# Performance work log

Measured on AMD Instinct MI355X. Metric: run time of the kernel, lower is better.

## Reference

```python
import jax, jax.numpy as jnp
import numpy as np

NP_, NA_, NS_ = 200000, 30000, 50000
D = 128          # embed_dim == hidden_dim
P = 128          # projection_dim
L = 3            # num GNN layers
R = 6            # num relations
LN_EPS = 1e-5
L2_EPS = 1e-12

# relation order matches metadata[1]: (src_type, dst_type, n_src, n_dst, n_edges)
RELS = [
    ("artist", "performance", NA_, NP_, 400000),      # performs
    ("performance", "song", NP_, NS_, 400000),        # performing
    ("artist", "song", NA_, NS_, 150000),             # composed
    ("performance", "artist", NP_, NA_, 400000),      # rev_performs
    ("song", "performance", NS_, NP_, 400000),        # rev_performing
    ("song", "artist", NS_, NA_, 150000),             # rev_composed
]
NNODES = {"performance": NP_, "artist": NA_, "song": NS_}


def _segment_mean(src, idx, n):
    # src: [E, D] messages, idx: [E] destination ids
    s = jax.ops.segment_sum(src, idx, num_segments=n)
    c = jax.ops.segment_sum(jnp.ones((src.shape[0], 1), src.dtype), idx, num_segments=n)
    return s / jnp.maximum(c, 1.0)


def _l2norm(x):
    n = jnp.linalg.norm(x, axis=-1, keepdims=True)
    return x / jnp.maximum(n, L2_EPS)


def _layernorm(x, g, b):
    mu = jnp.mean(x, axis=-1, keepdims=True)
    var = jnp.mean(jnp.square(x - mu), axis=-1, keepdims=True)
    return (x - mu) * jax.lax.rsqrt(var + LN_EPS) * g + b


def setup_inputs() -> dict:
    key = jax.random.key(0)
    ks = list(jax.random.split(key, 32))
    ki = iter(ks)
    inp = {}
    inp["perf_nid"] = jnp.arange(NP_, dtype=jnp.int32)
    inp["artist_nid"] = jnp.arange(NA_, dtype=jnp.int32)
    inp["song_nid"] = jnp.arange(NS_, dtype=jnp.int32)
    enames = ["e_performs", "e_performing", "e_composed",
              "e_rev_performs", "e_rev_performing", "e_rev_composed"]
    for name, (s, t, n_src, n_dst, n_e) in zip(enames, RELS):
        src = jax.random.randint(next(ki), (n_e,), 0, n_src, dtype=jnp.int32)
        dst = jax.random.randint(next(ki), (n_e,), 0, n_dst, dtype=jnp.int32)
        inp[name] = jnp.stack([src, dst])  # [2, E]
    inp["emb_performance"] = jax.random.normal(next(ki), (NP_, D), jnp.float32)
    inp["emb_artist"] = jax.random.normal(next(ki), (NA_, D), jnp.float32)
    inp["emb_song"] = jax.random.normal(next(ki), (NS_, D), jnp.float32)
    sc = 1.0 / np.sqrt(D)
    inp["Wl"] = jax.random.normal(next(ki), (L, R, D, D), jnp.float32) * sc
    inp["bl"] = jnp.zeros((L, R, D), jnp.float32)
    inp["Wr"] = jax.random.normal(next(ki), (L, R, D, D), jnp.float32) * sc
    inp["ln_g"] = jnp.ones((3, D), jnp.float32)
    inp["ln_b"] = jnp.zeros((3, D), jnp.float32)
    inp["pw1"] = jax.random.normal(next(ki), (3, D, P), jnp.float32) * sc
    inp["pb1"] = jnp.zeros((3, P), jnp.float32)
    inp["pw2"] = jax.random.normal(next(ki), (3, P, P), jnp.float32) * (1.0 / np.sqrt(P))
    inp["pb2"] = jnp.zeros((3, P), jnp.float32)
    return inp


def _forward(perf_nid, artist_nid, song_nid, edges,
             emb_performance, emb_artist, emb_song,
             Wl, bl, Wr, ln_g, ln_b, pw1, pb1, pw2, pb2):
    x = {
        "performance": emb_performance[perf_nid],
        "artist": emb_artist[artist_nid],
        "song": emb_song[song_nid],
    }
    for layer in range(L):
        new = {t: 0.0 for t in x}
        for r, ((s, t, _, _, _), e) in enumerate(zip(RELS, edges)):
            # SAGEConv: lin_l(mean_agg(x_src)) + lin_r(x_dst), then L2 normalize
            msg = _segment_mean(x[s][e[0]], e[1], x[t].shape[0])
            out = msg @ Wl[layer, r] + bl[layer, r] + x[t] @ Wr[layer, r]
            new[t] = new[t] + _l2norm(out)  # HeteroConv aggr='sum'
        x = new
        if layer < L - 1:
            x = {t: jax.nn.relu(v) for t, v in x.items()}
    res = []
    for i, t in enumerate(["performance", "artist", "song"]):
        h = _layernorm(x[t], ln_g[i], ln_b[i])
        h = jax.nn.relu(h @ pw1[i] + pb1[i]) @ pw2[i] + pb2[i]
        res.append(_l2norm(h))
    return tuple(res)


def reference(perf_nid, artist_nid, song_nid,
              e_performs, e_performing, e_composed,
              e_rev_performs, e_rev_performing, e_rev_composed,
              emb_performance, emb_artist, emb_song,
              Wl, bl, Wr, ln_g, ln_b, pw1, pb1, pw2, pb2):
    edges = [e_performs, e_performing, e_composed,
             e_rev_performs, e_rev_performing, e_rev_composed]
    return _forward(perf_nid, artist_nid, song_nid, edges,
                    emb_performance, emb_artist, emb_song,
                    Wl, bl, Wr, ln_g, ln_b, pw1, pb1, pw2, pb2)
```

## Files before the change

kernel.cpp:

```cpp
#include <hip/hip_runtime.h>
#include <math.h>


#define NPF 200000
#define NAR 30000
#define NSO 50000
#define NDTOT 560000
#define ETOT  1900000
#define VPT 12
#define SCAN_CHUNK (256 * VPT)
#define SCAN_NB 183

#define BLKP 3125
#define BLKA 469
#define BLKS 782
#define BLKTOT (BLKP + BLKA + BLKS)

typedef __attribute__((ext_vector_type(8))) short bf16x8;
typedef __attribute__((ext_vector_type(4))) float f32x4;

__device__ __forceinline__ unsigned short f2bf(float f) {
  union { float f; unsigned u; } v; v.f = f;
  unsigned u = v.u;
  u += 0x7FFFu + ((u >> 16) & 1u);
  return (unsigned short)(u >> 16);
}
__device__ __forceinline__ float bf2f(unsigned short h) {
  union { unsigned u; float f; } v; v.u = ((unsigned)h) << 16;
  return v.f;
}

struct BF3 { short h, m, l; };
__device__ __forceinline__ BF3 split3(float f) {
  BF3 r;
  unsigned short hh = f2bf(f);
  float r1 = f - bf2f(hh);
  unsigned short mm = f2bf(r1);
  float r2 = r1 - bf2f(mm);
  r.h = (short)hh; r.m = (short)mm; r.l = (short)f2bf(r2);
  return r;
}
struct BF2 { short h, m; };
__device__ __forceinline__ BF2 split2(float f) {
  BF2 r;
  unsigned short hh = f2bf(f);
  r.h = (short)hh;
  r.m = (short)f2bf(f - bf2f(hh));
  return r;
}

#define MFMA6(ah, am, al, bh, bm, blo, acc)                                     \
  acc = __builtin_amdgcn_mfma_f32_16x16x32_bf16(ah, bh, acc, 0, 0, 0);          \
  acc = __builtin_amdgcn_mfma_f32_16x16x32_bf16(am, bh, acc, 0, 0, 0);          \
  acc = __builtin_amdgcn_mfma_f32_16x16x32_bf16(ah, bm, acc, 0, 0, 0);          \
  acc = __builtin_amdgcn_mfma_f32_16x16x32_bf16(al, bh, acc, 0, 0, 0);          \
  acc = __builtin_amdgcn_mfma_f32_16x16x32_bf16(am, bm, acc, 0, 0, 0);          \
  acc = __builtin_amdgcn_mfma_f32_16x16x32_bf16(ah, blo, acc, 0, 0, 0);
#define MFMA3(ah, am, bh, bm, acc)                                              \
  acc = __builtin_amdgcn_mfma_f32_16x16x32_bf16(ah, bh, acc, 0, 0, 0);          \
  acc = __builtin_amdgcn_mfma_f32_16x16x32_bf16(am, bh, acc, 0, 0, 0);          \
  acc = __builtin_amdgcn_mfma_f32_16x16x32_bf16(ah, bm, acc, 0, 0, 0);

__device__ __forceinline__ void blk_decode(int b, int* t, int* lb) {
  if (b < BLKP)             { *t = 0; *lb = b; }
  else if (b < BLKP + BLKA) { *t = 1; *lb = b - BLKP; }
  else                      { *t = 2; *lb = b - BLKP - BLKA; }
}

__global__ void k_gather_all(const int* __restrict__ nidP, const int* __restrict__ nidA,
                             const int* __restrict__ nidS,
                             const float4* __restrict__ embP, const float4* __restrict__ embA,
                             const float4* __restrict__ embS, float4* __restrict__ dst) {
  int i = blockIdx.x * blockDim.x + threadIdx.x;
  if (i >= 280000 * 32) return;
  int r = i >> 5, c = i & 31;
  const int* nid; const float4* emb; int lr;
  if (r < NPF)            { nid = nidP; emb = embP; lr = r; }
  else if (r < NPF + NAR) { nid = nidA; emb = embA; lr = r - NPF; }
  else                    { nid = nidS; emb = embS; lr = r - NPF - NAR; }
  dst[(size_t)r * 32 + c] = emb[(size_t)nid[lr] * 32 + c];
}

__device__ __forceinline__ void edge_decode(int i,
    const int* e0, const int* e1, const int* e2, const int* e3, const int* e4, const int* e5,
    const int** eg, int* lo, int* E, int* co) {
  if (i < 400000)       { *eg = e0; *lo = i;           *E = 400000; *co = 0; }
  else if (i < 800000)  { *eg = e1; *lo = i - 400000;  *E = 400000; *co = 200000; }
  else if (i < 950000)  { *eg = e2; *lo = i - 800000;  *E = 150000; *co = 250000; }
  else if (i < 1350000) { *eg = e3; *lo = i - 950000;  *E = 400000; *co = 300000; }
  else if (i < 1750000) { *eg = e4; *lo = i - 1350000; *E = 400000; *co = 330000; }
  else                  { *eg = e5; *lo = i - 1750000; *E = 150000; *co = 530000; }
}

__global__ void k_count_all(const int* e0, const int* e1, const int* e2,
                            const int* e3, const int* e4, const int* e5,
                            int* __restrict__ cnt) {
  int i = blockIdx.x * blockDim.x + threadIdx.x;
  if (i >= ETOT) return;
  const int* eg; int lo, E, co;
  edge_decode(i, e0, e1, e2, e3, e4, e5, &eg, &lo, &E, &co);
  atomicAdd(&cnt[co + eg[E + lo]], 1);
}

__global__ void k_scan_block(const int* __restrict__ cnt, int n, int* __restrict__ part) {
  __shared__ int sd[256];
  int t = threadIdx.x;
  int base = blockIdx.x * SCAN_CHUNK + t * VPT;
  int s = 0;
#pragma unroll
  for (int i = 0; i < VPT; ++i) { int idx = base + i; if (idx < n) s += cnt[idx]; }
  sd[t] = s; __syncthreads();
  for (int off = 128; off > 0; off >>= 1) { if (t < off) sd[t] += sd[t + off]; __syncthreads(); }
  if (t == 0) part[blockIdx.x] = sd[0];
}

__global__ void k_scan_top(int* part, int nb) {
  __shared__ int sd[256];
  int t = threadIdx.x;
  int v = (t < nb) ? part[t] : 0;
  sd[t] = v; __syncthreads();
  for (int off = 1; off < 256; off <<= 1) {
    int add = (t >= off) ? sd[t - off] : 0;
    __syncthreads();
    sd[t] += add;
    __syncthreads();
  }
  if (t < nb) part[t] = sd[t] - v;
}

__global__ void k_scan_final(int* __restrict__ cnt, int n, const int* __restrict__ part,
                             int* __restrict__ rp, int E) {
  __shared__ int sd[256];
  int t = threadIdx.x;
  int base = blockIdx.x * SCAN_CHUNK + t * VPT;
  int v[VPT]; int s = 0;
#pragma unroll
  for (int i = 0; i < VPT; ++i) { int idx = base + i; v[i] = (idx < n) ? cnt[idx] : 0; s += v[i]; }
  sd[t] = s; __syncthreads();
  for (int off = 1; off < 256; off <<= 1) {
    int add = (t >= off) ? sd[t - off] : 0;
    __syncthreads();
    sd[t] += add;
    __syncthreads();
  }
  int run = part[blockIdx.x] + sd[t] - s;
#pragma unroll
  for (int i = 0; i < VPT; ++i) {
    int idx = base + i;
    if (idx < n) { rp[idx] = run; cnt[idx] = 0; }
    run += v[i];
  }
  if (blockIdx.x == 0 && t == 0) rp[n] = E;
}

__global__ void k_fill_all(const int* e0, const int* e1, const int* e2,
                           const int* e3, const int* e4, const int* e5,
                           const int* __restrict__ rp, int* __restrict__ cur,
                           int* __restrict__ col) {
  int i = blockIdx.x * blockDim.x + threadIdx.x;
  if (i >= ETOT) return;
  const int* eg; int lo, E, co;
  edge_decode(i, e0, e1, e2, e3, e4, e5, &eg, &lo, &E, &co);
  int d = co + eg[E + lo];
  int p = atomicAdd(&cur[d], 1);
  col[rp[d] + p] = eg[lo];
}

#define PKSTRIDE 49152
__global__ void k_packW(const float* __restrict__ Wl, const float* __restrict__ Wr,
                        const float* __restrict__ pw1, const float* __restrict__ pw2,
                        unsigned short* __restrict__ pk) {
  int gid = blockIdx.x * blockDim.x + threadIdx.x;
  if (gid >= 42 * 4 * 8 * 64) return;
  int lane = gid & 63;
  int t = (gid >> 6) & 7;
  int s = (gid >> 9) & 3;
  int m = gid >> 11;
  const float* src;
  if (m < 18) src = Wl + (size_t)m * 16384;
  else if (m < 36) src = Wr + (size_t)(m - 18) * 16384;
  else if (m < 39) src = pw1 + (size_t)(m - 36) * 16384;
  else src = pw2 + (size_t)(m - 39) * 16384;
  int n = t * 16 + (lane & 15);
  int k0 = s * 32 + (lane >> 4) * 8;
  unsigned short* hi = pk + (size_t)m * PKSTRIDE + ((size_t)(s * 8 + t) * 64 + lane) * 8;
  unsigned short* mid = hi + 16384;
  unsigned short* lo = hi + 32768;
#pragma unroll
  for (int j = 0; j < 8; ++j) {
    float f = src[(size_t)(k0 + j) * 128 + n];
    BF3 w = split3(f);
    hi[j] = (unsigned short)w.h;
    mid[j] = (unsigned short)w.m;
    lo[j] = (unsigned short)w.l;
  }
}

__global__ __launch_bounds__(256) void k_sage_merged(
    const int* __restrict__ rp, const int* __restrict__ col,
    const float* __restrict__ xin, float* __restrict__ xout,
    const unsigned short* __restrict__ pkw, const float* __restrict__ bl,
    int layer, int slot, int relu_out) {
  __shared__ float Ms[64 * 128];
  static const int RELSLOT[2][3] = {{0, 3, 1}, {4, 5, 2}};
  static const int SRCT[2][3]    = {{1, 0, 0}, {2, 2, 1}};
  static const int CNT_OFF[6] = {0, 200000, 250000, 300000, 330000, 530000};
  static const int TOFFc[3] = {0, NPF, NPF + NAR};
  static const int TNc[3]   = {NPF, NAR, NSO};
  int ty, lb;
  blk_decode(blockIdx.x, &ty, &lb);
  int rel = RELSLOT[slot][ty];
  int m = layer * 6 + rel;
  const int* rpt = rp + CNT_OFF[rel];
  const float* xsrc = xin + (size_t)TOFFc[SRCT[slot][ty]] * 128;
  const float* xdst = xin + (size_t)TOFFc[ty] * 128;
  float* outp = xout + (size_t)TOFFc[ty] * 128;
  const unsigned short* pkl = pkw + (size_t)m * PKSTRIDE;
  const unsigned short* pkr = pkw + (size_t)(18 + m) * PKSTRIDE;
  const float* blv = bl + (size_t)m * 128;
  int n_dst = TNc[ty];
  int first = (slot == 0);

  int lane = threadIdx.x & 63;
  int wave = threadIdx.x >> 6;
  int row0b = lb * 64;

  {
    int g = lane >> 4, li = lane & 15;
    int c0 = li * 8;
    int bb[4], ne[4];
    int maxd = 0;
#pragma unroll
    for (int i = 0; i < 4; ++i) {
      int d = row0b + wave * 16 + g * 4 + i;
      int b = 0, e = 0;
      if (d < n_dst) { b = rpt[d]; e = rpt[d + 1]; }
      bb[i] = b; ne[i] = e - b;
      maxd = max(maxd, e - b);
    }
    f32x4 a0[4], a1[4];
#pragma unroll
    for (int i = 0; i < 4; ++i) { a0[i] = (f32x4){0.f,0.f,0.f,0.f}; a1[i] = (f32x4){0.f,0.f,0.f,0.f}; }
    int nc[4];
#pragma unroll
    for (int i = 0; i < 4; ++i) nc[i] = (0 < ne[i]) ? col[bb[i]] : 0;
    for (int k = 0; k < maxd; ++k) {
      int cc[4];
#pragma unroll
      for (int i = 0; i < 4; ++i) cc[i] = nc[i];
#pragma unroll
      for (int i = 0; i < 4; ++i) nc[i] = (k + 1 < ne[i]) ? col[bb[i] + k + 1] : 0;
#pragma unroll
      for (int i = 0; i < 4; ++i) {
        if (k < ne[i]) {
          const float* sp = xsrc + (size_t)cc[i] * 128 + c0;
          float4 v0 = *(const float4*)sp;
          float4 v1 = *(const float4*)(sp + 4);
          a0[i][0] += v0.x; a0[i][1] += v0.y; a0[i][2] += v0.z; a0[i][3] += v0.w;
          a1[i][0] += v1.x; a1[i][1] += v1.y; a1[i][2] += v1.z; a1[i][3] += v1.w;
        }
      }
    }
#pragma unroll
    for (int i = 0; i < 4; ++i) {
      float inv = (ne[i] > 0) ? 1.0f / (float)ne[i] : 0.0f;
      int lr = wave * 16 + g * 4 + i;
      float4* Mrow = (float4*)&Ms[lr * 128];
      int sw = lr & 7;
      Mrow[(li * 2) ^ sw]     = make_float4(a0[i][0]*inv, a0[i][1]*inv, a0[i][2]*inv, a0[i][3]*inv);
      Mrow[(li * 2 + 1) ^ sw] = make_float4(a1[i][0]*inv, a1[i][1]*inv, a1[i][2]*inv, a1[i][3]*inv);
    }
  }

  int row0 = row0b + wave * 16;
  int cg = lane & 15, qg = lane >> 4;
  int ar = min(row0 + cg, n_dst - 1);
  int lar = wave * 16 + cg;
  int kb = qg * 8;
  const float4* Mlar = (const float4*)&Ms[lar * 128];
  int swl = lar & 7;

  f32x4 acc[8];
#pragma unroll
  for (int t = 0; t < 8; ++t) acc[t] = (f32x4){0.f, 0.f, 0.f, 0.f};

#pragma unroll
  for (int sm = 0; sm < 2; ++sm) {
    const unsigned short* pk = sm ? pkr : pkl;
#pragma unroll
    for (int s = 0; s < 4; ++s) {
      float4 f0, f1;
      if (sm) {
        const float* ap = xdst + (size_t)ar * 128 + s * 32 + kb;
        f0 = *(const float4*)ap;
        f1 = *(const float4*)(ap + 4);
      } else {
        int ch = s * 8 + qg * 2;
        f0 = Mlar[ch ^ swl];
        f1 = Mlar[(ch + 1) ^ swl];
      }
      float fa[8] = {f0.x, f0.y, f0.z, f0.w, f1.x, f1.y, f1.z, f1.w};
      bf16x8 ah, am;
#pragma unroll
      for (int j = 0; j < 8; ++j) {
        BF2 w = split2(fa[j]);
        ah[j] = w.h; am[j] = w.m;
      }
      const unsigned short* pb = pk + (size_t)s * 4096 + (size_t)lane * 8;
#pragma unroll
      for (int t = 0; t < 8; ++t) {
        bf16x8 bh = *(const bf16x8*)(pb + (size_t)t * 512);
        bf16x8 bm = *(const bf16x8*)(pb + (size_t)t * 512 + 16384);
        MFMA3(ah, am, bh, bm, acc[t]);
      }
    }
  }

#pragma unroll
  for (int t = 0; t < 8; ++t) {
    float bv = blv[t * 16 + cg];
#pragma unroll
    for (int j = 0; j < 4; ++j) acc[t][j] += bv;
  }
  float ss[4];
#pragma unroll
  for (int j = 0; j < 4; ++j) {
    float s = 0.f;
#pragma unroll
    for (int t = 0; t < 8; ++t) s += acc[t][j] * acc[t][j];
    s += __shfl_xor(s, 1); s += __shfl_xor(s, 2);
    s += __shfl_xor(s, 4); s += __shfl_xor(s, 8);
    ss[j] = 1.0f / fmaxf(sqrtf(s), 1e-12f);
  }
#pragma unroll
  for (int j = 0; j < 4; ++j) {
    int r = row0 + qg * 4 + j;
    if (r < n_dst) {
      float* p = outp + (size_t)r * 128 + cg;
      if (first) {
#pragma unroll
        for (int t = 0; t < 8; ++t) p[t * 16] = acc[t][j] * ss[j];
      } else {
#pragma unroll
        for (int t = 0; t < 8; ++t) {
          float v = p[t * 16] + acc[t][j] * ss[j];
          if (relu_out) v = fmaxf(v, 0.f);
          p[t * 16] = v;
        }
      }
    }
  }
}

__global__ __launch_bounds__(256) void k_ln_all(const float* __restrict__ in,
                                                float* __restrict__ out,
                                                const float* __restrict__ lng,
                                                const float* __restrict__ lnb) {
  int gid = blockIdx.x * blockDim.x + threadIdx.x;
  int r = gid >> 2, q = gid & 3;
  if (r >= NPF + NAR + NSO) return;
  int ty = (r < NPF) ? 0 : ((r < NPF + NAR) ? 1 : 2);
  const float* g = lng + ty * 128;
  const float* bvec = lnb + ty * 128;
  float v[32];
#pragma unroll
  for (int j = 0; j < 8; ++j) {
    float4 t4 = *(const float4*)(in + (size_t)r * 128 + q * 32 + j * 4);
    v[4 * j] = t4.x; v[4 * j + 1] = t4.y; v[4 * j + 2] = t4.z; v[4 * j + 3] = t4.w;
  }
  float s = 0.f, sq = 0.f;
#pragma unroll
  for (int j = 0; j < 32; ++j) { s += v[j]; sq += v[j] * v[j]; }
  s  += __shfl_xor(s, 1);  s  += __shfl_xor(s, 2);
  sq += __shfl_xor(sq, 1); sq += __shfl_xor(sq, 2);
  float mu = s * 0.0078125f;
  float var = sq * 0.0078125f - mu * mu;
  float rs = rsqrtf(var + 1e-5f);
#pragma unroll
  for (int j = 0; j < 8; ++j) {
    float o[4];
#pragma unroll
    for (int k = 0; k < 4; ++k) {
      int c = q * 32 + j * 4 + k;
      o[k] = (v[j * 4 + k] - mu) * rs * g[c] + bvec[c];
    }
    *(float4*)(out + (size_t)r * 128 + q * 32 + j * 4) = make_float4(o[0], o[1], o[2], o[3]);
  }
}

__global__ __launch_bounds__(256) void k_gemm_all(
    const float* __restrict__ A, const unsigned short* __restrict__ pkw,
    const float* __restrict__ biasb, float* __restrict__ outp,
    int pkbase, int relu, int l2n) {
  static const int TOFFc[3] = {0, NPF, NPF + NAR};
  static const int TNc[3]   = {NPF, NAR, NSO};
  int ty, lb;
  blk_decode(blockIdx.x, &ty, &lb);
  const unsigned short* pk = pkw + (size_t)(pkbase + ty) * PKSTRIDE;
  const float* bias = biasb + ty * 128;
  const float* At = A + (size_t)TOFFc[ty] * 128;
  float* outt = outp + (size_t)TOFFc[ty] * 128;
  int n = TNc[ty];

  int lane = threadIdx.x & 63;
  int wave = threadIdx.x >> 6;
  int row0 = lb * 64 + wave * 16;
  int cg = lane & 15, qg = lane >> 4;
  int ar = min(row0 + cg, n - 1);
  int kb = qg * 8;

  f32x4 acc[8];
#pragma unroll
  for (int t = 0; t < 8; ++t) acc[t] = (f32x4){0.f, 0.f, 0.f, 0.f};

#pragma unroll
  for (int s = 0; s < 4; ++s) {
    const float* ap = At + (size_t)ar * 128 + s * 32 + kb;
    float4 f0 = *(const float4*)ap;
    float4 f1 = *(const float4*)(ap + 4);
    float fa[8] = {f0.x, f0.y, f0.z, f0.w, f1.x, f1.y, f1.z, f1.w};
    bf16x8 ah, am, al;
#pragma unroll
    for (int j = 0; j < 8; ++j) {
      BF3 w = split3(fa[j]);
      ah[j] = w.h; am[j] = w.m; al[j] = w.l;
    }
    const unsigned short* pb = pk + (size_t)s * 4096 + (size_t)lane * 8;
#pragma unroll
    for (int t = 0; t < 8; ++t) {
      bf16x8 bh  = *(const bf16x8*)(pb + (size_t)t * 512);
      bf16x8 bm  = *(const bf16x8*)(pb + (size_t)t * 512 + 16384);
      bf16x8 blo = *(const bf16x8*)(pb + (size_t)t * 512 + 32768);
      MFMA6(ah, am, al, bh, bm, blo, acc[t]);
    }
  }

#pragma unroll
  for (int t = 0; t < 8; ++t) {
    float bv = bias[t * 16 + cg];
#pragma unroll
    for (int j = 0; j < 4; ++j) acc[t][j] += bv;
  }

  float ss[4];
  if (l2n) {
#pragma unroll
    for (int j = 0; j < 4; ++j) {
      float s = 0.f;
#pragma unroll
      for (int t = 0; t < 8; ++t) s += acc[t][j] * acc[t][j];
      s += __shfl_xor(s, 1); s += __shfl_xor(s, 2);
      s += __shfl_xor(s, 4); s += __shfl_xor(s, 8);
      ss[j] = 1.0f / fmaxf(sqrtf(s), 1e-12f);
    }
  } else {
#pragma unroll
    for (int j = 0; j < 4; ++j) ss[j] = 1.0f;
  }

#pragma unroll
  for (int j = 0; j < 4; ++j) {
    int r = row0 + qg * 4 + j;
    if (r < n) {
      float* p = outt + (size_t)r * 128 + cg;
#pragma unroll
      for (int t = 0; t < 8; ++t) {
        float v = acc[t][j] * ss[j];
        if (relu) v = fmaxf(v, 0.f);
        p[t * 16] = v;
      }
    }
  }
}

extern "C" void kernel_launch(void* const* d_in, const int* in_sizes, int n_in,
                              void* d_out, int out_size, void* d_ws, size_t ws_size,
                              hipStream_t stream) {
  const int* nid[3] = {(const int*)d_in[0], (const int*)d_in[1], (const int*)d_in[2]};
  const int* eg[6];
  for (int r = 0; r < 6; ++r) eg[r] = (const int*)d_in[3 + r];
  const float* emb[3] = {(const float*)d_in[9], (const float*)d_in[10], (const float*)d_in[11]};
  const float* Wl  = (const float*)d_in[12];
  const float* bl  = (const float*)d_in[13];
  const float* Wr  = (const float*)d_in[14];
  const float* lng = (const float*)d_in[15];
  const float* lnb = (const float*)d_in[16];
  const float* pw1 = (const float*)d_in[17];
  const float* pb1 = (const float*)d_in[18];
  const float* pw2 = (const float*)d_in[19];
  const float* pb2 = (const float*)d_in[20];

  float* cur = (float*)d_ws;
  int* col   = (int*)(cur + (size_t)280000 * 128);
  int* rp    = col + ETOT;
  int* cnt   = rp + NDTOT + 1;
  int* part  = cnt + NDTOT;
  size_t pk_off = ((size_t)((char*)(part + 256) - (char*)d_ws) + 255) & ~(size_t)255;
  unsigned short* pkw = (unsigned short*)((char*)d_ws + pk_off);
  float* dout = (float*)d_out;

  k_packW<<<dim3(336), dim3(256), 0, stream>>>(Wl, Wr, pw1, pw2, pkw);

  k_gather_all<<<dim3((280000 * 32 + 255) / 256), dim3(256), 0, stream>>>(
      nid[0], nid[1], nid[2],
      (const float4*)emb[0], (const float4*)emb[1], (const float4*)emb[2],
      (float4*)cur);

  hipMemsetAsync(cnt, 0, (size_t)NDTOT * 4, stream);
  k_count_all<<<dim3((ETOT + 255) / 256), dim3(256), 0, stream>>>(
      eg[0], eg[1], eg[2], eg[3], eg[4], eg[5], cnt);
  k_scan_block<<<dim3(SCAN_NB), dim3(256), 0, stream>>>(cnt, NDTOT, part);
  k_scan_top<<<dim3(1), dim3(256), 0, stream>>>(part, SCAN_NB);
  k_scan_final<<<dim3(SCAN_NB), dim3(256), 0, stream>>>(cnt, NDTOT, part, rp, ETOT);
  k_fill_all<<<dim3((ETOT + 255) / 256), dim3(256), 0, stream>>>(
      eg[0], eg[1], eg[2], eg[3], eg[4], eg[5], rp, cnt, col);

  for (int layer = 0; layer < 3; ++layer) {
    float* xin  = (layer == 1) ? dout : cur;
    float* xout = (layer == 1) ? cur  : dout;
    int relu_o = (layer < 2) ? 1 : 0;
    k_sage_merged<<<dim3(BLKTOT), dim3(256), 0, stream>>>(
        rp, col, xin, xout, pkw, bl, layer, 0, relu_o);
    k_sage_merged<<<dim3(BLKTOT), dim3(256), 0, stream>>>(
        rp, col, xin, xout, pkw, bl, layer, 1, relu_o);
  }

  k_ln_all<<<dim3((280000 * 4 + 255) / 256), dim3(256), 0, stream>>>(
      dout, cur, lng, lnb);
  k_gemm_all<<<dim3(BLKTOT), dim3(256), 0, stream>>>(
      cur, pkw, pb1, cur, 36, 1, 0);
  k_gemm_all<<<dim3(BLKTOT), dim3(256), 0, stream>>>(
      cur, pkw, pb2, dout, 39, 0, 1);

  (void)in_sizes; (void)n_in; (void)out_size; (void)ws_size;
}
```

Baseline: 1.811 ms.

## Fuse both relation passes into one SAGE kernel and use bf16x2 projection GEMM

Each destination type's two incoming relations are now processed inside one kernel launch per layer. The L2-normalized outputs are summed in registers and written once, replacing the old first-pass write followed by a second-pass read-modify-write of the whole output. The projection head GEMM also drops from a 3-way bf16 split with 6 MFMAs to a 2-way split with 3 MFMAs, halving its matrix work and weight loads at some cost in precision. The extra register accumulator may lower occupancy in the merged kernel.

```diff
diff --git a/kernel.cpp b/kernel.cpp
--- a/kernel.cpp
+++ b/kernel.cpp
@@ -49,13 +49,6 @@
   return r;
 }
 
-#define MFMA6(ah, am, al, bh, bm, blo, acc)                                     \
-  acc = __builtin_amdgcn_mfma_f32_16x16x32_bf16(ah, bh, acc, 0, 0, 0);          \
-  acc = __builtin_amdgcn_mfma_f32_16x16x32_bf16(am, bh, acc, 0, 0, 0);          \
-  acc = __builtin_amdgcn_mfma_f32_16x16x32_bf16(ah, bm, acc, 0, 0, 0);          \
-  acc = __builtin_amdgcn_mfma_f32_16x16x32_bf16(al, bh, acc, 0, 0, 0);          \
-  acc = __builtin_amdgcn_mfma_f32_16x16x32_bf16(am, bm, acc, 0, 0, 0);          \
-  acc = __builtin_amdgcn_mfma_f32_16x16x32_bf16(ah, blo, acc, 0, 0, 0);
 #define MFMA3(ah, am, bh, bm, acc)                                              \
   acc = __builtin_amdgcn_mfma_f32_16x16x32_bf16(ah, bh, acc, 0, 0, 0);          \
   acc = __builtin_amdgcn_mfma_f32_16x16x32_bf16(am, bh, acc, 0, 0, 0);          \
@@ -196,11 +189,11 @@
   }
 }
 
-__global__ __launch_bounds__(256) void k_sage_merged(
+__global__ __launch_bounds__(256) void k_sage_merged2(
     const int* __restrict__ rp, const int* __restrict__ col,
     const float* __restrict__ xin, float* __restrict__ xout,
     const unsigned short* __restrict__ pkw, const float* __restrict__ bl,
-    int layer, int slot, int relu_out) {
+    int layer, int relu_out) {
   __shared__ float Ms[64 * 128];
   static const int RELSLOT[2][3] = {{0, 3, 1}, {4, 5, 2}};
   static const int SRCT[2][3]    = {{1, 0, 0}, {2, 2, 1}};
@@ -209,69 +202,13 @@
   static const int TNc[3]   = {NPF, NAR, NSO};
   int ty, lb;
   blk_decode(blockIdx.x, &ty, &lb);
-  int rel = RELSLOT[slot][ty];
-  int m = layer * 6 + rel;
-  const int* rpt = rp + CNT_OFF[rel];
-  const float* xsrc = xin + (size_t)TOFFc[SRCT[slot][ty]] * 128;
   const float* xdst = xin + (size_t)TOFFc[ty] * 128;
   float* outp = xout + (size_t)TOFFc[ty] * 128;
-  const unsigned short* pkl = pkw + (size_t)m * PKSTRIDE;
-  const unsigned short* pkr = pkw + (size_t)(18 + m) * PKSTRIDE;
-  const float* blv = bl + (size_t)m * 128;
   int n_dst = TNc[ty];
-  int first = (slot == 0);
 
   int lane = threadIdx.x & 63;
   int wave = threadIdx.x >> 6;
   int row0b = lb * 64;
-
-  {
-    int g = lane >> 4, li = lane & 15;
-    int c0 = li * 8;
-    int bb[4], ne[4];
-    int maxd = 0;
-#pragma unroll
-    for (int i = 0; i < 4; ++i) {
-      int d = row0b + wave * 16 + g * 4 + i;
-      int b = 0, e = 0;
-      if (d < n_dst) { b = rpt[d]; e = rpt[d + 1]; }
-      bb[i] = b; ne[i] = e - b;
-      maxd = max(maxd, e - b);
-    }
-    f32x4 a0[4], a1[4];
-#pragma unroll
-    for (int i = 0; i < 4; ++i) { a0[i] = (f32x4){0.f,0.f,0.f,0.f}; a1[i] = (f32x4){0.f,0.f,0.f,0.f}; }
-    int nc[4];
-#pragma unroll
-    for (int i = 0; i < 4; ++i) nc[i] = (0 < ne[i]) ? col[bb[i]] : 0;
-    for (int k = 0; k < maxd; ++k) {
-      int cc[4];
-#pragma unroll
-      for (int i = 0; i < 4; ++i) cc[i] = nc[i];
-#pragma unroll
-      for (int i = 0; i < 4; ++i) nc[i] = (k + 1 < ne[i]) ? col[bb[i] + k + 1] : 0;
-#pragma unroll
-      for (int i = 0; i < 4; ++i) {
-        if (k < ne[i]) {
-          const float* sp = xsrc + (size_t)cc[i] * 128 + c0;
-          float4 v0 = *(const float4*)sp;
-          float4 v1 = *(const float4*)(sp + 4);
-          a0[i][0] += v0.x; a0[i][1] += v0.y; a0[i][2] += v0.z; a0[i][3] += v0.w;
-          a1[i][0] += v1.x; a1[i][1] += v1.y; a1[i][2] += v1.z; a1[i][3] += v1.w;
-        }
-      }
-    }
-#pragma unroll
-    for (int i = 0; i < 4; ++i) {
-      float inv = (ne[i] > 0) ? 1.0f / (float)ne[i] : 0.0f;
-      int lr = wave * 16 + g * 4 + i;
-      float4* Mrow = (float4*)&Ms[lr * 128];
-      int sw = lr & 7;
-      Mrow[(li * 2) ^ sw]     = make_float4(a0[i][0]*inv, a0[i][1]*inv, a0[i][2]*inv, a0[i][3]*inv);
-      Mrow[(li * 2 + 1) ^ sw] = make_float4(a1[i][0]*inv, a1[i][1]*inv, a1[i][2]*inv, a1[i][3]*inv);
-    }
-  }
-
   int row0 = row0b + wave * 16;
   int cg = lane & 15, qg = lane >> 4;
   int ar = min(row0 + cg, n_dst - 1);
@@ -280,73 +217,132 @@
   const float4* Mlar = (const float4*)&Ms[lar * 128];
   int swl = lar & 7;
 
-  f32x4 acc[8];
-#pragma unroll
-  for (int t = 0; t < 8; ++t) acc[t] = (f32x4){0.f, 0.f, 0.f, 0.f};
-
-#pragma unroll
-  for (int sm = 0; sm < 2; ++sm) {
-    const unsigned short* pk = sm ? pkr : pkl;
-#pragma unroll
-    for (int s = 0; s < 4; ++s) {
-      float4 f0, f1;
-      if (sm) {
-        const float* ap = xdst + (size_t)ar * 128 + s * 32 + kb;
-        f0 = *(const float4*)ap;
-        f1 = *(const float4*)(ap + 4);
-      } else {
-        int ch = s * 8 + qg * 2;
-        f0 = Mlar[ch ^ swl];
-        f1 = Mlar[(ch + 1) ^ swl];
+  f32x4 o[8];
+#pragma unroll
+  for (int t = 0; t < 8; ++t) o[t] = (f32x4){0.f, 0.f, 0.f, 0.f};
+
+#pragma unroll 1
+  for (int r2 = 0; r2 < 2; ++r2) {
+    int rel = RELSLOT[r2][ty];
+    int m = layer * 6 + rel;
+    const int* rpt = rp + CNT_OFF[rel];
+    const float* xsrc = xin + (size_t)TOFFc[SRCT[r2][ty]] * 128;
+    const unsigned short* pkl = pkw + (size_t)m * PKSTRIDE;
+    const unsigned short* pkr = pkw + (size_t)(18 + m) * PKSTRIDE;
+    const float* blv = bl + (size_t)m * 128;
+
+    {
+      int g = lane >> 4, li = lane & 15;
+      int c0 = li * 8;
+      int bb[4], ne[4];
+      int maxd = 0;
+#pragma unroll
+      for (int i = 0; i < 4; ++i) {
+        int d = row0b + wave * 16 + g * 4 + i;
+        int b = 0, e = 0;
+        if (d < n_dst) { b = rpt[d]; e = rpt[d + 1]; }
+        bb[i] = b; ne[i] = e - b;
+        maxd = max(maxd, e - b);
       }
-      float fa[8] = {f0.x, f0.y, f0.z, f0.w, f1.x, f1.y, f1.z, f1.w};
-      bf16x8 ah, am;
-#pragma unroll
-      for (int j = 0; j < 8; ++j) {
-        BF2 w = split2(fa[j]);
-        ah[j] = w.h; am[j] = w.m;
+      f32x4 a0[4], a1[4];
+#pragma unroll
+      for (int i = 0; i < 4; ++i) { a0[i] = (f32x4){0.f,0.f,0.f,0.f}; a1[i] = (f32x4){0.f,0.f,0.f,0.f}; }
+      int nc[4];
+#pragma unroll
+      for (int i = 0; i < 4; ++i) nc[i] = (0 < ne[i]) ? col[bb[i]] : 0;
+      for (int k = 0; k < maxd; ++k) {
+        int cc[4];
+#pragma unroll
+        for (int i = 0; i < 4; ++i) cc[i] = nc[i];
+#pragma unroll
+        for (int i = 0; i < 4; ++i) nc[i] = (k + 1 < ne[i]) ? col[bb[i] + k + 1] : 0;
+#pragma unroll
+        for (int i = 0; i < 4; ++i) {
+          if (k < ne[i]) {
+            const float* sp = xsrc + (size_t)cc[i] * 128 + c0;
+            float4 v0 = *(const float4*)sp;
+            float4 v1 = *(const float4*)(sp + 4);
+            a0[i][0] += v0.x; a0[i][1] += v0.y; a0[i][2] += v0.z; a0[i][3] += v0.w;
+            a1[i][0] += v1.x; a1[i][1] += v1.y; a1[i][2] += v1.z; a1[i][3] += v1.w;
+          }
+        }
       }
-      const unsigned short* pb = pk + (size_t)s * 4096 + (size_t)lane * 8;
-#pragma unroll
-      for (int t = 0; t < 8; ++t) {
-        bf16x8 bh = *(const bf16x8*)(pb + (size_t)t * 512);
-        bf16x8 bm = *(const bf16x8*)(pb + (size_t)t * 512 + 16384);
-        MFMA3(ah, am, bh, bm, acc[t]);
+#pragma unroll
+      for (int i = 0; i < 4; ++i) {
+        float inv = (ne[i] > 0) ? 1.0f / (float)ne[i] : 0.0f;
+        int lr = wave * 16 + g * 4 + i;
+        float4* Mrow = (float4*)&Ms[lr * 128];
+        int sw = lr & 7;
+        Mrow[(li * 2) ^ sw]     = make_float4(a0[i][0]*inv, a0[i][1]*inv, a0[i][2]*inv, a0[i][3]*inv);
+        Mrow[(li * 2 + 1) ^ sw] = make_float4(a1[i][0]*inv, a1[i][1]*inv, a1[i][2]*inv, a1[i][3]*inv);
       }
     }
-  }
-
-#pragma unroll
-  for (int t = 0; t < 8; ++t) {
-    float bv = blv[t * 16 + cg];
-#pragma unroll
-    for (int j = 0; j < 4; ++j) acc[t][j] += bv;
-  }
-  float ss[4];
-#pragma unroll
-  for (int j = 0; j < 4; ++j) {
-    float s = 0.f;
-#pragma unroll
-    for (int t = 0; t < 8; ++t) s += acc[t][j] * acc[t][j];
-    s += __shfl_xor(s, 1); s += __shfl_xor(s, 2);
-    s += __shfl_xor(s, 4); s += __shfl_xor(s, 8);
-    ss[j] = 1.0f / fmaxf(sqrtf(s), 1e-12f);
-  }
+
+    f32x4 acc[8];
+#pragma unroll
+    for (int t = 0; t < 8; ++t) acc[t] = (f32x4){0.f, 0.f, 0.f, 0.f};
+
+#pragma unroll
+    for (int sm = 0; sm < 2; ++sm) {
+      const unsigned short* pk = sm ? pkr : pkl;
+#pragma unroll
+      for (int s = 0; s < 4; ++s) {
+        float4 f0, f1;
+        if (sm) {
+          const float* ap = xdst + (size_t)ar * 128 + s * 32 + kb;
+          f0 = *(const float4*)ap;
+          f1 = *(const float4*)(ap + 4);
+        } else {
+          int ch = s * 8 + qg * 2;
+          f0 = Mlar[ch ^ swl];
+          f1 = Mlar[(ch + 1) ^ swl];
+        }
+        float fa[8] = {f0.x, f0.y, f0.z, f0.w, f1.x, f1.y, f1.z, f1.w};
+        bf16x8 ah, am;
+#pragma unroll
+        for (int j = 0; j < 8; ++j) {
+          BF2 w = split2(fa[j]);
+          ah[j] = w.h; am[j] = w.m;
+        }
+        const unsigned short* pb = pk + (size_t)s * 4096 + (size_t)lane * 8;
+#pragma unroll
+        for (int t = 0; t < 8; ++t) {
+          bf16x8 bh = *(const bf16x8*)(pb + (size_t)t * 512);
+          bf16x8 bm = *(const bf16x8*)(pb + (size_t)t * 512 + 16384);
+          MFMA3(ah, am, bh, bm, acc[t]);
+        }
+      }
+    }
+
+#pragma unroll
+    for (int t = 0; t < 8; ++t) {
+      float bv = blv[t * 16 + cg];
+#pragma unroll
+      for (int j = 0; j < 4; ++j) acc[t][j] += bv;
+    }
+#pragma unroll
+    for (int j = 0; j < 4; ++j) {
+      float s = 0.f;
+#pragma unroll
+      for (int t = 0; t < 8; ++t) s += acc[t][j] * acc[t][j];
+      s += __shfl_xor(s, 1); s += __shfl_xor(s, 2);
+      s += __shfl_xor(s, 4); s += __shfl_xor(s, 8);
+      float sc = 1.0f / fmaxf(sqrtf(s), 1e-12f);
+#pragma unroll
+      for (int t = 0; t < 8; ++t) o[t][j] += acc[t][j] * sc;
+    }
+  }
+
 #pragma unroll
   for (int j = 0; j < 4; ++j) {
     int r = row0 + qg * 4 + j;
     if (r < n_dst) {
       float* p = outp + (size_t)r * 128 + cg;
-      if (first) {
-#pragma unroll
-        for (int t = 0; t < 8; ++t) p[t * 16] = acc[t][j] * ss[j];
-      } else {
-#pragma unroll
-        for (int t = 0; t < 8; ++t) {
-          float v = p[t * 16] + acc[t][j] * ss[j];
-          if (relu_out) v = fmaxf(v, 0.f);
-          p[t * 16] = v;
-        }
+#pragma unroll
+      for (int t = 0; t < 8; ++t) {
+        float v = o[t][j];
+        if (relu_out) v = fmaxf(v, 0.f);
+        p[t * 16] = v;
       }
     }
   }
@@ -419,19 +415,18 @@
     float4 f0 = *(const float4*)ap;
     float4 f1 = *(const float4*)(ap + 4);
     float fa[8] = {f0.x, f0.y, f0.z, f0.w, f1.x, f1.y, f1.z, f1.w};
-    bf16x8 ah, am, al;
+    bf16x8 ah, am;
 #pragma unroll
     for (int j = 0; j < 8; ++j) {
-      BF3 w = split3(fa[j]);
-      ah[j] = w.h; am[j] = w.m; al[j] = w.l;
+      BF2 w = split2(fa[j]);
+      ah[j] = w.h; am[j] = w.m;
     }
     const unsigned short* pb = pk + (size_t)s * 4096 + (size_t)lane * 8;
 #pragma unroll
     for (int t = 0; t < 8; ++t) {
-      bf16x8 bh  = *(const bf16x8*)(pb + (size_t)t * 512);
-      bf16x8 bm  = *(const bf16x8*)(pb + (size_t)t * 512 + 16384);
-      bf16x8 blo = *(const bf16x8*)(pb + (size_t)t * 512 + 32768);
-      MFMA6(ah, am, al, bh, bm, blo, acc[t]);
+      bf16x8 bh = *(const bf16x8*)(pb + (size_t)t * 512);
+      bf16x8 bm = *(const bf16x8*)(pb + (size_t)t * 512 + 16384);
+      MFMA3(ah, am, bh, bm, acc[t]);
     }
   }
 
@@ -519,10 +514,8 @@
     float* xin  = (layer == 1) ? dout : cur;
     float* xout = (layer == 1) ? cur  : dout;
     int relu_o = (layer < 2) ? 1 : 0;
-    k_sage_merged<<<dim3(BLKTOT), dim3(256), 0, stream>>>(
-        rp, col, xin, xout, pkw, bl, layer, 0, relu_o);
-    k_sage_merged<<<dim3(BLKTOT), dim3(256), 0, stream>>>(
-        rp, col, xin, xout, pkw, bl, layer, 1, relu_o);
+    k_sage_merged2<<<dim3(BLKTOT), dim3(256), 0, stream>>>(
+        rp, col, xin, xout, pkw, bl, layer, relu_o);
   }
 
   k_ln_all<<<dim3((280000 * 4 + 255) / 256), dim3(256), 0, stream>>>(
```

After: 1.838 ms. Within noise of the previous version (+1.5%).
